# Kernel tuning notes

Measured on AMD Instinct MI355X. Metric: run time of the kernel, lower is better.

## Reference

```python
import jax, jax.numpy as jnp
import numpy as np

MULTI_INFER_NUM = 8
D_EMBED = 128
N_LAYERS = 2
T, B = 2048, 32


def setup_inputs() -> dict:
    key = jax.random.key(0)
    k1, k2, k3, k4 = jax.random.split(key, 4)
    positions = jax.random.randint(k1, (T, B), 0, 16, dtype=jnp.int64)
    outputs = jax.random.normal(k2, (T, B, D_EMBED), dtype=jnp.float32)
    # 4 LinearTransferFeatures per layer (self_forget, logit, logit_forget, out_forget)
    Ws = jax.random.normal(k3, (N_LAYERS, 4, MULTI_INFER_NUM + 1, D_EMBED, D_EMBED), dtype=jnp.float32) * 0.05
    bs = jax.random.normal(k4, (N_LAYERS, 4, MULTI_INFER_NUM + 1, D_EMBED), dtype=jnp.float32) * 0.05
    return {"positions": positions, "outputs": outputs, "Ws": Ws, "bs": bs}


def _linear(x, onehot, W, b):
    # x: [t,b,d]; onehot: [t,b,e]; W: [e,d,f]; b: [e,d]
    # Equivalent to gathering W[r_pos] ([t,b,d,f]) then einsum('ibde,ibd->ibe'),
    # but computed as per-expert GEMMs + one-hot combine (grouped-GEMM form).
    y_all = jnp.einsum('tbd,edf->tbef', x, W)      # per-expert outputs
    y = jnp.einsum('tbef,tbe->tbf', y_all, onehot)  # select token's expert
    return y + jnp.einsum('tbe,ed->tbd', onehot, b)


def reference(positions, outputs, Ws, bs):
    m = Ws.shape[2] - 1  # multi_infer_num
    r_pos = jnp.where(positions < m, positions, m)
    onehot = jax.nn.one_hot(r_pos, m + 1, dtype=outputs.dtype)
    x = outputs
    for l in range(Ws.shape[0]):
        self_forget = _linear(x, onehot, Ws[l, 0], bs[l, 0])
        logit = _linear(x, onehot, Ws[l, 1], bs[l, 1])
        logit_forget = _linear(x, onehot, Ws[l, 2], bs[l, 2])
        out_forget = _linear(x, onehot, Ws[l, 3], bs[l, 3])
        new_res = x * jax.nn.sigmoid(self_forget) + jnp.tanh(logit) * jax.nn.sigmoid(logit_forget)
        x = jnp.tanh(new_res) * jax.nn.sigmoid(out_forget)
    return x
```

## Files before the change

### kernel.cpp

```cpp
#include <hip/hip_runtime.h>
#include <hip/hip_fp16.h>
#include <stdint.h>

#define TOKENS 65536
#define D      128
#define NEXP   9
#define MT     32
#define MAXTILES (TOKENS / MT + NEXP)
#define NHB    256

typedef _Float16 f16;
typedef _Float16 f16x8  __attribute__((ext_vector_type(8)));
typedef float    f32x4  __attribute__((ext_vector_type(4)));
typedef uint32_t u32;

#define WI_TOKOFF  32
#define WI_TILEOFF 48
#define WI_HIST    128
#define WI_BBASE   2432
#define WI_PERM    4736
#define WS_WF_OFF  ((4736 + TOKENS) * 4)

#define LOG2E  1.44269504f
__device__ __forceinline__ float sigm(float v) {
  return __builtin_amdgcn_rcpf(1.0f + __builtin_amdgcn_exp2f(-LOG2E * v));
}
__device__ __forceinline__ float tanh_fast(float v) {
  return 1.0f - 2.0f * __builtin_amdgcn_rcpf(__builtin_amdgcn_exp2f(2.0f * LOG2E * v) + 1.0f);
}

__global__ void k_prep(const float* __restrict__ Ws, const int* __restrict__ pos,
                       int* __restrict__ wsI, f16* __restrict__ Wf) {
  const int tid = threadIdx.x;
  if (blockIdx.x < 288) {
    const int mat = blockIdx.x >> 2;
    const int q   = blockIdx.x & 3;
    const float* src = Ws + (size_t)mat * (D * D);
    f16* dst = Wf + (size_t)mat * (D * D);
#pragma unroll
    for (int p = 0; p < 2; ++p) {
      int cc = q * 512 + p * 256 + tid;
      int ln = cc & 63;
      int kb = (cc >> 6) & 3;
      int c  = cc >> 8;
      int quad = ln >> 4, n = ln & 15;
      int f  = c * 16 + n;
      int d0 = kb * 32 + quad * 8;
      f16x8 w;
#pragma unroll
      for (int i = 0; i < 8; ++i) w[i] = (f16)src[(d0 + i) * D + f];
      *(f16x8*)(dst + cc * 8) = w;
    }
  } else {
    const int b = blockIdx.x - 288;
    __shared__ int h[NEXP];
    if (tid < NEXP) h[tid] = 0;
    __syncthreads();
    int e = pos[b * 256 + tid]; e = e < 8 ? e : 8;
    atomicAdd(&h[e], 1);
    __syncthreads();
    if (tid < NEXP) wsI[WI_HIST + b * NEXP + tid] = h[tid];
  }
}

__global__ void k_scan(int* __restrict__ wsI) {
  const int tid = threadIdx.x;
  const int lane = tid & 63, w = tid >> 6;
  __shared__ int wsum[4];
  __shared__ int totalsS[NEXP];
  __shared__ int tokoffS[NEXP + 1];
  int rel[NEXP];
  int myh[NEXP];
#pragma unroll
  for (int e = 0; e < NEXP; ++e) myh[e] = wsI[WI_HIST + tid * NEXP + e];

  for (int e = 0; e < NEXP; ++e) {
    int v = myh[e];
    int x = v;
#pragma unroll
    for (int off = 1; off < 64; off <<= 1) {
      int y = __shfl_up(x, off);
      if (lane >= off) x += y;
    }
    if (lane == 63) wsum[w] = x;
    __syncthreads();
    int add = 0;
    for (int w2 = 0; w2 < w; ++w2) add += wsum[w2];
    int incl = x + add;
    rel[e] = incl - v;
    if (tid == 255) totalsS[e] = incl;
    __syncthreads();
  }
  if (tid == 0) {
    int tok = 0, tile = 0;
    wsI[WI_TOKOFF] = 0; wsI[WI_TILEOFF] = 0; tokoffS[0] = 0;
    for (int e = 0; e < NEXP; ++e) {
      int cnt = totalsS[e];
      tok += cnt; tile += (cnt + MT - 1) / MT;
      wsI[WI_TOKOFF + e + 1] = tok;  tokoffS[e + 1] = tok;
      wsI[WI_TILEOFF + e + 1] = tile;
    }
  }
  __syncthreads();
#pragma unroll
  for (int e = 0; e < NEXP; ++e)
    wsI[WI_BBASE + tid * NEXP + e] = tokoffS[e] + rel[e];
}

__global__ void k_assign(const int* __restrict__ pos, int* __restrict__ wsI) {
  const int tid = threadIdx.x, b = blockIdx.x;
  const int lane = tid & 63, w = tid >> 6;
  int e = pos[b * 256 + tid]; e = e < 8 ? e : 8;
  __shared__ int waveCnt[4][NEXP];
  __shared__ int waveBase[4][NEXP];
  int myRank = 0;
#pragma unroll
  for (int ee = 0; ee < NEXP; ++ee) {
    unsigned long long m = __ballot(e == ee);
    if (e == ee) myRank = __popcll(m & ((1ull << lane) - 1ull));
    if (lane == 0) waveCnt[w][ee] = __popcll(m);
  }
  __syncthreads();
  if (tid < NEXP) {
    int s = 0;
#pragma unroll
    for (int w2 = 0; w2 < 4; ++w2) { waveBase[w2][tid] = s; s += waveCnt[w2][tid]; }
  }
  __syncthreads();
  int base = wsI[WI_BBASE + b * NEXP + e];
  wsI[WI_PERM + base + waveBase[w][e] + myRank] = b * 256 + tid;
}

__launch_bounds__(256, 4)
__global__ void k_main(const float* __restrict__ xin, const float* __restrict__ bsPtr,
                       const int* __restrict__ wsI, const f16* __restrict__ Wf,
                       float* __restrict__ outPtr) {
  __shared__ __attribute__((aligned(16))) f16 Ash[MT][136];
  __shared__ int s_tok[MT];

  const int tid = threadIdx.x;
  const int bid = blockIdx.x;
  const int ntiles = wsI[WI_TILEOFF + NEXP];
  if (bid >= ntiles) return;

  int e = 0, tileOffE = 0;
#pragma unroll
  for (int ee = 0; ee < NEXP; ee++) {
    int to = wsI[WI_TILEOFF + ee];
    if (to <= bid) { e = ee; tileOffE = to; }
  }
  const int tokStart = wsI[WI_TOKOFF + e] + (bid - tileOffE) * MT;
  const int tokEnd   = wsI[WI_TOKOFF + e + 1];
  const int rowsValid = min(MT, tokEnd - tokStart);

  {
    int m = tid >> 3, h = tid & 7;
    bool valid = (m < rowsValid);
    int tok = 0;
    if (valid) tok = wsI[WI_PERM + tokStart + m];
    if (h == 0) s_tok[m] = valid ? tok : -1;
    const float4* src = (const float4*)(xin + (size_t)tok * D + h * 16);
    f16* drow = &Ash[m][h * 16];
#pragma unroll
    for (int i = 0; i < 2; i++) {
      float4 a = make_float4(0.f, 0.f, 0.f, 0.f), b2 = a;
      if (valid) { a = src[2 * i]; b2 = src[2 * i + 1]; }
      f16x8 wv;
      wv[0] = (f16)a.x;  wv[1] = (f16)a.y;  wv[2] = (f16)a.z;  wv[3] = (f16)a.w;
      wv[4] = (f16)b2.x; wv[5] = (f16)b2.y; wv[6] = (f16)b2.z; wv[7] = (f16)b2.w;
      *(f16x8*)&drow[i * 8] = wv;
    }
  }
  __syncthreads();

  const int lane = tid & 63;
  const int n    = lane & 15;
  const int quad = lane >> 4;
  const int cBase = (tid >> 6) * 2;
  const int vlane = lane * 8;
  const f16* We = Wf + (size_t)e * 16384;

  f16x8 aF0[4], aF1[4];
  f16x8 b0[4], b1[4];
  f32x4 acc[4][2];

#define LOAD_AF()                                                              \
  do {                                                                         \
    _Pragma("unroll")                                                          \
    for (int _kb = 0; _kb < 4; ++_kb) {                                        \
      aF0[_kb] = *(const f16x8*)&Ash[n][_kb * 32 + quad * 8];                  \
      aF1[_kb] = *(const f16x8*)&Ash[16 + n][_kb * 32 + quad * 8];             \
    }                                                                          \
  } while (0)

#define PREFETCH_B(BUF, LL, CC, JJ)                                            \
  do {                                                                         \
    if ((LL) < 2) {                                                            \
      const f16* _p = We + ((LL) * 4 + (JJ)) * 147456 + (CC) * 2048 + vlane;   \
      _Pragma("unroll")                                                        \
      for (int _kb = 0; _kb < 4; ++_kb)                                        \
        BUF[_kb] = *(const f16x8*)(_p + _kb * 512);                            \
    }                                                                          \
  } while (0)

#define MFMA2(G, BUF)                                                          \
  do {                                                                         \
    f32x4 _x = {0.f, 0.f, 0.f, 0.f}, _y = {0.f, 0.f, 0.f, 0.f};                \
    _Pragma("unroll")                                                          \
    for (int _kb = 0; _kb < 4; ++_kb) {                                        \
      _x = __builtin_amdgcn_mfma_f32_16x16x32_f16(aF0[_kb], BUF[_kb], _x, 0, 0, 0); \
      _y = __builtin_amdgcn_mfma_f32_16x16x32_f16(aF1[_kb], BUF[_kb], _y, 0, 0, 0); \
    }                                                                          \
    acc[G][0] = _x; acc[G][1] = _y;                                            \
  } while (0)

  PREFETCH_B(b0, 0, cBase, 0);
  LOAD_AF();
  __syncthreads();

#pragma unroll 1
  for (int l = 0; l < 2; l++) {
#pragma unroll 1
    for (int ci = 0; ci < 2; ci++) {
      const int cc = cBase + ci;
      const int f = cc * 16 + n;
      float bias[4];
#pragma unroll
      for (int j = 0; j < 4; j++)
        bias[j] = bsPtr[((l * 4 + j) * NEXP + e) * D + f];

      const int ln = (ci == 1) ? l + 1 : l;
      const int cn = (ci == 1) ? cBase : cc + 1;

      PREFETCH_B(b1, l, cc, 1);  MFMA2(0, b0);
      PREFETCH_B(b0, l, cc, 2);  MFMA2(1, b1);
      PREFETCH_B(b1, l, cc, 3);  MFMA2(2, b0);
      PREFETCH_B(b0, ln, cn, 0); MFMA2(3, b1);

#pragma unroll
      for (int s = 0; s < 2; s++) {
#pragma unroll
        for (int r = 0; r < 4; r++) {
          int m = s * 16 + quad * 4 + r;
          float sf = acc[0][s][r] + bias[0];
          float lg = acc[1][s][r] + bias[1];
          float lf = acc[2][s][r] + bias[2];
          float of = acc[3][s][r] + bias[3];
          float xv = (float)Ash[m][f];
          float nr = xv * sigm(sf) + tanh_fast(lg) * sigm(lf);
          float xn = tanh_fast(nr) * sigm(of);
          if (l == 0) {
            Ash[m][f] = (f16)xn;
          } else {
            int tok = s_tok[m];
            if (tok >= 0) outPtr[(size_t)tok * D + f] = xn;
          }
        }
      }
    }
    if (l == 0) {
      __syncthreads();
      LOAD_AF();
    }
  }
#undef LOAD_AF
#undef PREFETCH_B
#undef MFMA2
}

extern "C" void kernel_launch(void* const* d_in, const int* in_sizes, int n_in,
                              void* d_out, int out_size, void* d_ws, size_t ws_size,
                              hipStream_t stream) {
  const int*   pos = (const int*)d_in[0];
  const float* x   = (const float*)d_in[1];
  const float* Ws  = (const float*)d_in[2];
  const float* bs  = (const float*)d_in[3];
  float* out = (float*)d_out;
  int* wsI = (int*)d_ws;
  f16* Wf = (f16*)((char*)d_ws + WS_WF_OFF);

  k_prep  <<<544, 256, 0, stream>>>(Ws, pos, wsI, Wf);
  k_scan  <<<1, 256, 0, stream>>>(wsI);
  k_assign<<<NHB, 256, 0, stream>>>(pos, wsI);
  k_main  <<<MAXTILES, 256, 0, stream>>>(x, bs, wsI, Wf, out);
}
```

Baseline: 132.5 us.

## Fuse scan into assign, preload all weights per chunk, stage biases in LDS, fold activations

Merges the single-block scan kernel into the assign kernel: each of the 256 blocks redundantly recomputes the global histogram scan, which removes one launch and the per-block base buffer. In the main kernel, all 16 weight fragments for a column chunk are loaded into registers up front, the matmuls run at raised wave priority, and the next chunk is prefetched after the MFMAs. The biases for the expert are staged in shared memory. The sigmoid/tanh gate math is rewritten with fewer reciprocals. Occupancy hint drops from 4 to 3 waves per SIMD because of the higher register use.

```diff
diff --git a/kernel.cpp b/kernel.cpp
--- a/kernel.cpp
+++ b/kernel.cpp
@@ -17,17 +17,10 @@
 #define WI_TOKOFF  32
 #define WI_TILEOFF 48
 #define WI_HIST    128
-#define WI_BBASE   2432
 #define WI_PERM    4736
 #define WS_WF_OFF  ((4736 + TOKENS) * 4)
 
 #define LOG2E  1.44269504f
-__device__ __forceinline__ float sigm(float v) {
-  return __builtin_amdgcn_rcpf(1.0f + __builtin_amdgcn_exp2f(-LOG2E * v));
-}
-__device__ __forceinline__ float tanh_fast(float v) {
-  return 1.0f - 2.0f * __builtin_amdgcn_rcpf(__builtin_amdgcn_exp2f(2.0f * LOG2E * v) + 1.0f);
-}
 
 __global__ void k_prep(const float* __restrict__ Ws, const int* __restrict__ pos,
                        int* __restrict__ wsI, f16* __restrict__ Wf) {
@@ -63,13 +56,18 @@
   }
 }
 
-__global__ void k_scan(int* __restrict__ wsI) {
-  const int tid = threadIdx.x;
+__global__ void k_scan_assign(const int* __restrict__ pos, int* __restrict__ wsI) {
+  const int tid = threadIdx.x, b = blockIdx.x;
   const int lane = tid & 63, w = tid >> 6;
   __shared__ int wsum[4];
-  __shared__ int totalsS[NEXP];
-  __shared__ int tokoffS[NEXP + 1];
-  int rel[NEXP];
+  __shared__ int totS[NEXP];
+  __shared__ int relB[NEXP];
+  __shared__ int baseS[NEXP];
+  __shared__ int waveCnt[4][NEXP];
+  __shared__ int waveBase[4][NEXP];
+
+  int myE = pos[b * 256 + tid]; myE = myE < 8 ? myE : 8;
+
   int myh[NEXP];
 #pragma unroll
   for (int e = 0; e < NEXP; ++e) myh[e] = wsI[WI_HIST + tid * NEXP + e];
@@ -87,37 +85,25 @@
     int add = 0;
     for (int w2 = 0; w2 < w; ++w2) add += wsum[w2];
     int incl = x + add;
-    rel[e] = incl - v;
-    if (tid == 255) totalsS[e] = incl;
+    if (tid == b)   relB[e] = incl - v;
+    if (tid == 255) totS[e] = incl;
     __syncthreads();
   }
   if (tid == 0) {
     int tok = 0, tile = 0;
-    wsI[WI_TOKOFF] = 0; wsI[WI_TILEOFF] = 0; tokoffS[0] = 0;
+    if (b == 0) { wsI[WI_TOKOFF] = 0; wsI[WI_TILEOFF] = 0; }
     for (int e = 0; e < NEXP; ++e) {
-      int cnt = totalsS[e];
+      baseS[e] = tok + relB[e];
+      int cnt = totS[e];
       tok += cnt; tile += (cnt + MT - 1) / MT;
-      wsI[WI_TOKOFF + e + 1] = tok;  tokoffS[e + 1] = tok;
-      wsI[WI_TILEOFF + e + 1] = tile;
-    }
-  }
-  __syncthreads();
-#pragma unroll
-  for (int e = 0; e < NEXP; ++e)
-    wsI[WI_BBASE + tid * NEXP + e] = tokoffS[e] + rel[e];
-}
-
-__global__ void k_assign(const int* __restrict__ pos, int* __restrict__ wsI) {
-  const int tid = threadIdx.x, b = blockIdx.x;
-  const int lane = tid & 63, w = tid >> 6;
-  int e = pos[b * 256 + tid]; e = e < 8 ? e : 8;
-  __shared__ int waveCnt[4][NEXP];
-  __shared__ int waveBase[4][NEXP];
+      if (b == 0) { wsI[WI_TOKOFF + e + 1] = tok; wsI[WI_TILEOFF + e + 1] = tile; }
+    }
+  }
   int myRank = 0;
 #pragma unroll
   for (int ee = 0; ee < NEXP; ++ee) {
-    unsigned long long m = __ballot(e == ee);
-    if (e == ee) myRank = __popcll(m & ((1ull << lane) - 1ull));
+    unsigned long long m = __ballot(myE == ee);
+    if (myE == ee) myRank = __popcll(m & ((1ull << lane) - 1ull));
     if (lane == 0) waveCnt[w][ee] = __popcll(m);
   }
   __syncthreads();
@@ -127,15 +113,15 @@
     for (int w2 = 0; w2 < 4; ++w2) { waveBase[w2][tid] = s; s += waveCnt[w2][tid]; }
   }
   __syncthreads();
-  int base = wsI[WI_BBASE + b * NEXP + e];
-  wsI[WI_PERM + base + waveBase[w][e] + myRank] = b * 256 + tid;
-}
-
-__launch_bounds__(256, 4)
+  wsI[WI_PERM + baseS[myE] + waveBase[w][myE] + myRank] = b * 256 + tid;
+}
+
+__launch_bounds__(256, 3)
 __global__ void k_main(const float* __restrict__ xin, const float* __restrict__ bsPtr,
                        const int* __restrict__ wsI, const f16* __restrict__ Wf,
                        float* __restrict__ outPtr) {
   __shared__ __attribute__((aligned(16))) f16 Ash[MT][136];
+  __shared__ float Bsh[8][D];
   __shared__ int s_tok[MT];
 
   const int tid = threadIdx.x;
@@ -152,6 +138,41 @@
   const int tokStart = wsI[WI_TOKOFF + e] + (bid - tileOffE) * MT;
   const int tokEnd   = wsI[WI_TOKOFF + e + 1];
   const int rowsValid = min(MT, tokEnd - tokStart);
+
+  const int lane = tid & 63;
+  const int n    = lane & 15;
+  const int quad = lane >> 4;
+  const int cBase = (tid >> 6) * 2;
+  const int vlane = lane * 8;
+  const f16* We = Wf + (size_t)e * 16384;
+
+  f16x8 bb[16];
+#define LOADB(LL, CC)                                                          \
+  do {                                                                         \
+    const f16* _base = We + (size_t)(LL) * 4 * 147456 + (CC) * 2048 + vlane;   \
+    _Pragma("unroll")                                                          \
+    for (int _j = 0; _j < 4; ++_j)                                             \
+      _Pragma("unroll")                                                        \
+      for (int _kb = 0; _kb < 4; ++_kb)                                        \
+        bb[_j * 4 + _kb] = *(const f16x8*)(_base + _j * 147456 + _kb * 512);   \
+  } while (0)
+
+#define LOAD_AF()                                                              \
+  do {                                                                         \
+    _Pragma("unroll")                                                          \
+    for (int _kb = 0; _kb < 4; ++_kb) {                                        \
+      aF0[_kb] = *(const f16x8*)&Ash[n][_kb * 32 + quad * 8];                  \
+      aF1[_kb] = *(const f16x8*)&Ash[16 + n][_kb * 32 + quad * 8];             \
+    }                                                                          \
+  } while (0)
+
+  LOADB(0, cBase);
+
+  {
+    int mat = tid >> 5, d = (tid & 31) * 4;
+    float4 bv = *(const float4*)(bsPtr + (size_t)(mat * NEXP + e) * D + d);
+    *(float4*)&Bsh[mat][d] = bv;
+  }
 
   {
     int m = tid >> 3, h = tid & 7;
@@ -173,82 +194,65 @@
   }
   __syncthreads();
 
-  const int lane = tid & 63;
-  const int n    = lane & 15;
-  const int quad = lane >> 4;
-  const int cBase = (tid >> 6) * 2;
-  const int vlane = lane * 8;
-  const f16* We = Wf + (size_t)e * 16384;
-
   f16x8 aF0[4], aF1[4];
-  f16x8 b0[4], b1[4];
-  f32x4 acc[4][2];
-
-#define LOAD_AF()                                                              \
-  do {                                                                         \
-    _Pragma("unroll")                                                          \
-    for (int _kb = 0; _kb < 4; ++_kb) {                                        \
-      aF0[_kb] = *(const f16x8*)&Ash[n][_kb * 32 + quad * 8];                  \
-      aF1[_kb] = *(const f16x8*)&Ash[16 + n][_kb * 32 + quad * 8];             \
-    }                                                                          \
-  } while (0)
-
-#define PREFETCH_B(BUF, LL, CC, JJ)                                            \
-  do {                                                                         \
-    if ((LL) < 2) {                                                            \
-      const f16* _p = We + ((LL) * 4 + (JJ)) * 147456 + (CC) * 2048 + vlane;   \
-      _Pragma("unroll")                                                        \
-      for (int _kb = 0; _kb < 4; ++_kb)                                        \
-        BUF[_kb] = *(const f16x8*)(_p + _kb * 512);                            \
-    }                                                                          \
-  } while (0)
-
-#define MFMA2(G, BUF)                                                          \
-  do {                                                                         \
-    f32x4 _x = {0.f, 0.f, 0.f, 0.f}, _y = {0.f, 0.f, 0.f, 0.f};                \
-    _Pragma("unroll")                                                          \
-    for (int _kb = 0; _kb < 4; ++_kb) {                                        \
-      _x = __builtin_amdgcn_mfma_f32_16x16x32_f16(aF0[_kb], BUF[_kb], _x, 0, 0, 0); \
-      _y = __builtin_amdgcn_mfma_f32_16x16x32_f16(aF1[_kb], BUF[_kb], _y, 0, 0, 0); \
-    }                                                                          \
-    acc[G][0] = _x; acc[G][1] = _y;                                            \
-  } while (0)
-
-  PREFETCH_B(b0, 0, cBase, 0);
   LOAD_AF();
   __syncthreads();
+
+  const int f0 = cBase * 16 + n;
 
 #pragma unroll 1
   for (int l = 0; l < 2; l++) {
-#pragma unroll 1
+#pragma unroll
     for (int ci = 0; ci < 2; ci++) {
-      const int cc = cBase + ci;
-      const int f = cc * 16 + n;
-      float bias[4];
-#pragma unroll
-      for (int j = 0; j < 4; j++)
-        bias[j] = bsPtr[((l * 4 + j) * NEXP + e) * D + f];
-
-      const int ln = (ci == 1) ? l + 1 : l;
-      const int cn = (ci == 1) ? cBase : cc + 1;
-
-      PREFETCH_B(b1, l, cc, 1);  MFMA2(0, b0);
-      PREFETCH_B(b0, l, cc, 2);  MFMA2(1, b1);
-      PREFETCH_B(b1, l, cc, 3);  MFMA2(2, b0);
-      PREFETCH_B(b0, ln, cn, 0); MFMA2(3, b1);
+      const int f = f0 + ci * 16;
+
+      f32x4 acc[4][2];
+      __builtin_amdgcn_s_setprio(1);
+#pragma unroll
+      for (int j = 0; j < 4; ++j) {
+        f32x4 x0 = {0.f, 0.f, 0.f, 0.f}, x1 = {0.f, 0.f, 0.f, 0.f};
+#pragma unroll
+        for (int kb = 0; kb < 4; ++kb) {
+          x0 = __builtin_amdgcn_mfma_f32_16x16x32_f16(aF0[kb], bb[j * 4 + kb], x0, 0, 0, 0);
+          x1 = __builtin_amdgcn_mfma_f32_16x16x32_f16(aF1[kb], bb[j * 4 + kb], x1, 0, 0, 0);
+        }
+        acc[j][0] = x0; acc[j][1] = x1;
+      }
+      __builtin_amdgcn_s_setprio(0);
+
+      if (ci == 0)      LOADB(l, cBase + 1);
+      else if (l == 0)  LOADB(1, cBase);
+
+      float bv0 = Bsh[l * 4 + 0][f];
+      float bv1 = Bsh[l * 4 + 1][f];
+      float bv2 = Bsh[l * 4 + 2][f];
+      float bv3 = Bsh[l * 4 + 3][f];
+      float xv[2][4];
+#pragma unroll
+      for (int s = 0; s < 2; s++)
+#pragma unroll
+        for (int r = 0; r < 4; r++)
+          xv[s][r] = (float)Ash[s * 16 + quad * 4 + r][f];
 
 #pragma unroll
       for (int s = 0; s < 2; s++) {
 #pragma unroll
         for (int r = 0; r < 4; r++) {
           int m = s * 16 + quad * 4 + r;
-          float sf = acc[0][s][r] + bias[0];
-          float lg = acc[1][s][r] + bias[1];
-          float lf = acc[2][s][r] + bias[2];
-          float of = acc[3][s][r] + bias[3];
-          float xv = (float)Ash[m][f];
-          float nr = xv * sigm(sf) + tanh_fast(lg) * sigm(lf);
-          float xn = tanh_fast(nr) * sigm(of);
+          float sf = acc[0][s][r] + bv0;
+          float lg = acc[1][s][r] + bv1;
+          float lf = acc[2][s][r] + bv2;
+          float of = acc[3][s][r] + bv3;
+          float Ea = __builtin_amdgcn_exp2f(-LOG2E * sf);
+          float Eb = __builtin_amdgcn_exp2f((2.0f * LOG2E) * lg);
+          float Ec = __builtin_amdgcn_exp2f(-LOG2E * lf);
+          float d1 = 1.0f + Ea, d2 = Eb + 1.0f, d3 = 1.0f + Ec;
+          float p23 = d2 * d3;
+          float nr = (xv[s][r] * p23 + (Eb - 1.0f) * d1) *
+                     __builtin_amdgcn_rcpf(d1 * p23);
+          float Ed = __builtin_amdgcn_exp2f((2.0f * LOG2E) * nr);
+          float Ee = __builtin_amdgcn_exp2f(-LOG2E * of);
+          float xn = (Ed - 1.0f) * __builtin_amdgcn_rcpf((Ed + 1.0f) * (1.0f + Ee));
           if (l == 0) {
             Ash[m][f] = (f16)xn;
           } else {
@@ -263,9 +267,8 @@
       LOAD_AF();
     }
   }
+#undef LOADB
 #undef LOAD_AF
-#undef PREFETCH_B
-#undef MFMA2
 }
 
 extern "C" void kernel_launch(void* const* d_in, const int* in_sizes, int n_in,
@@ -279,8 +282,7 @@
   int* wsI = (int*)d_ws;
   f16* Wf = (f16*)((char*)d_ws + WS_WF_OFF);
 
-  k_prep  <<<544, 256, 0, stream>>>(Ws, pos, wsI, Wf);
-  k_scan  <<<1, 256, 0, stream>>>(wsI);
-  k_assign<<<NHB, 256, 0, stream>>>(pos, wsI);
-  k_main  <<<MAXTILES, 256, 0, stream>>>(x, bs, wsI, Wf, out);
-}
+  k_prep       <<<544, 256, 0, stream>>>(Ws, pos, wsI, Wf);
+  k_scan_assign<<<NHB, 256, 0, stream>>>(pos, wsI);
+  k_main       <<<MAXTILES, 256, 0, stream>>>(x, bs, wsI, Wf, out);
+}
```

After: 142.3 us. 1.07x slower.
